# Kernel optimization log

Hardware: AMD Instinct MI355X
Metric: run time of the kernel (lower is better)

The kernel has to match this reference:

```python
import jax, jax.numpy as jnp
import numpy as np

THRESH = 0.5
TAU = 0.5
GAMMA = 1.0
BETA = 0.9
A = 0.5
B = 0.5


def zif_spike(v):
    # ZIF surrogate: forward is hard threshold (v > 0).
    return (v > 0).astype(v.dtype)


def setup_inputs() -> dict:
    key = jax.random.key(0)
    x = jax.random.normal(key, (64, 8192, 100), dtype=jnp.float32)
    return {"x": x}


def reference(x):
    # x: [B, N, T]; scan over time with (mem, w) state kept per element.
    xt = jnp.moveaxis(x, 2, 0)  # [T, B, N]
    init_mem = jnp.zeros(xt.shape[1:], dtype=x.dtype)
    init_w = jnp.zeros(xt.shape[1:], dtype=x.dtype)

    def step(carry, x_t):
        mem, w = carry
        mem = mem * TAU + x_t - w
        spike = zif_spike(mem - THRESH)
        w = BETA * w + (1.0 - BETA) * (A * mem + B * spike)
        mem = mem - spike * THRESH  # soft reset
        return (mem, w), spike

    _, spikes = jax.lax.scan(step, (init_mem, init_w), xt)  # [T, B, N]
    return jnp.moveaxis(spikes, 0, 2)  # [B, N, T]
```

## Files before the change

kernel.cpp:

```cpp
#include <hip/hip_runtime.h>

#define T_STEPS 100
#define CHUNKS  25
#define TPB     64
#define ELEMS   64

__global__ __launch_bounds__(TPB) void lif_kernel(const float* __restrict__ x,
                                                  float* __restrict__ out) {
#pragma clang fp contract(off)
    __shared__ float4 tile[ELEMS * CHUNKS];

    const int lane = threadIdx.x;
    const size_t tile4 = (size_t)blockIdx.x * (ELEMS * CHUNKS);
    const float4* __restrict__ xp = (const float4*)x + tile4 + (size_t)lane * CHUNKS;
    float4* __restrict__ ob = (float4*)out + tile4;

    float4 xs[CHUNKS];
#pragma unroll
    for (int c = 0; c < CHUNKS; ++c) xs[c] = xp[c];

    {
        float mem = 0.0f;
        float w = 0.0f;
#pragma unroll
        for (int c = 0; c < CHUNKS; ++c) {
            float xv[4] = {xs[c].x, xs[c].y, xs[c].z, xs[c].w};
            float sv[4];
#pragma unroll
            for (int j = 0; j < 4; ++j) {
                mem = (mem * 0.5f + xv[j]) - w;
                float spike = (mem - 0.5f) > 0.0f ? 1.0f : 0.0f;
                w = 0.9f * w + 0.1f * (0.5f * mem + 0.5f * spike);
                mem = mem - spike * 0.5f;
                sv[j] = spike;
            }
            xs[c].x = sv[0]; xs[c].y = sv[1]; xs[c].z = sv[2]; xs[c].w = sv[3];
        }
    }

#pragma unroll
    for (int c = 0; c < CHUNKS; ++c) tile[lane * CHUNKS + c] = xs[c];
    __syncthreads();
#pragma unroll
    for (int k = 0; k < CHUNKS; ++k) {
        float4 s = tile[k * TPB + lane];
        ob[k * TPB + lane] = s;
    }
}

extern "C" void kernel_launch(void* const* d_in, const int* in_sizes, int n_in,
                              void* d_out, int out_size, void* d_ws, size_t ws_size,
                              hipStream_t stream) {
    const float* x = (const float*)d_in[0];
    float* out = (float*)d_out;
    int n_elem = in_sizes[0] / T_STEPS;
    int grid = n_elem / ELEMS;

    lif_kernel<<<grid, TPB, 0, stream>>>(x, out);
}
```

Measured before the change: 346.4 us.

## Use persistent grid-stride blocks with packed spike bytes in double-buffered LDS

The kernel now launches a fixed grid of 2048 blocks that loop over tiles in grid-stride fashion. Spikes are packed as bytes into a uint32 per chunk and written to a double-buffered shared array, which cuts LDS footprint and traffic fourfold. Values are unpacked to floats on the coalesced store. The aim is to cut shared-memory use and raise occupancy, and to amortize block launch. In exchange there are fewer blocks in flight and one barrier per tile, with the double buffer standing in for a second barrier.

```diff
diff --git a/kernel.cpp b/kernel.cpp
--- a/kernel.cpp
+++ b/kernel.cpp
@@ -4,47 +4,57 @@
 #define CHUNKS  25
 #define TPB     64
 #define ELEMS   64
+#define GRID    2048
 
 __global__ __launch_bounds__(TPB) void lif_kernel(const float* __restrict__ x,
-                                                  float* __restrict__ out) {
+                                                  float* __restrict__ out,
+                                                  int ntiles) {
 #pragma clang fp contract(off)
-    __shared__ float4 tile[ELEMS * CHUNKS];
+    __shared__ unsigned int sp[2][ELEMS * CHUNKS];
 
     const int lane = threadIdx.x;
-    const size_t tile4 = (size_t)blockIdx.x * (ELEMS * CHUNKS);
-    const float4* __restrict__ xp = (const float4*)x + tile4 + (size_t)lane * CHUNKS;
-    float4* __restrict__ ob = (float4*)out + tile4;
+    int parity = 0;
 
-    float4 xs[CHUNKS];
+    for (int t = blockIdx.x; t < ntiles; t += GRID, parity ^= 1) {
+        unsigned int* buf = sp[parity];
+        const size_t tile4 = (size_t)t * (ELEMS * CHUNKS);
+        const float4* __restrict__ xp = (const float4*)x + tile4 + (size_t)lane * CHUNKS;
+        float4* __restrict__ ob = (float4*)out + tile4;
+
+        float4 xs[CHUNKS];
 #pragma unroll
-    for (int c = 0; c < CHUNKS; ++c) xs[c] = xp[c];
+        for (int c = 0; c < CHUNKS; ++c) xs[c] = xp[c];
 
-    {
         float mem = 0.0f;
         float w = 0.0f;
 #pragma unroll
         for (int c = 0; c < CHUNKS; ++c) {
             float xv[4] = {xs[c].x, xs[c].y, xs[c].z, xs[c].w};
-            float sv[4];
+            unsigned int pack = 0;
 #pragma unroll
             for (int j = 0; j < 4; ++j) {
                 mem = (mem * 0.5f + xv[j]) - w;
-                float spike = (mem - 0.5f) > 0.0f ? 1.0f : 0.0f;
+                bool b = (mem - 0.5f) > 0.0f;
+                float spike = b ? 1.0f : 0.0f;
                 w = 0.9f * w + 0.1f * (0.5f * mem + 0.5f * spike);
                 mem = mem - spike * 0.5f;
-                sv[j] = spike;
+                pack |= b ? (1u << (8 * j)) : 0u;
             }
-            xs[c].x = sv[0]; xs[c].y = sv[1]; xs[c].z = sv[2]; xs[c].w = sv[3];
+            buf[lane * CHUNKS + c] = pack;
         }
-    }
+
+        __syncthreads();
 
 #pragma unroll
-    for (int c = 0; c < CHUNKS; ++c) tile[lane * CHUNKS + c] = xs[c];
-    __syncthreads();
-#pragma unroll
-    for (int k = 0; k < CHUNKS; ++k) {
-        float4 s = tile[k * TPB + lane];
-        ob[k * TPB + lane] = s;
+        for (int k = 0; k < CHUNKS; ++k) {
+            unsigned int p = buf[k * TPB + lane];
+            float4 s;
+            s.x = (float)(p & 0xffu);
+            s.y = (float)((p >> 8) & 0xffu);
+            s.z = (float)((p >> 16) & 0xffu);
+            s.w = (float)(p >> 24);
+            ob[k * TPB + lane] = s;
+        }
     }
 }
 
@@ -54,7 +64,7 @@
     const float* x = (const float*)d_in[0];
     float* out = (float*)d_out;
     int n_elem = in_sizes[0] / T_STEPS;
-    int grid = n_elem / ELEMS;
+    int ntiles = n_elem / ELEMS;
 
-    lif_kernel<<<grid, TPB, 0, stream>>>(x, out);
+    lif_kernel<<<GRID, TPB, 0, stream>>>(x, out, ntiles);
 }
```

Result: no change. 350.1 us (+1.1%).
